# Optimization experiments

Measured on AMD Instinct MI355X. Metric: run time of the kernel, lower is better.

Reference implementation:

```python
import jax, jax.numpy as jnp
import numpy as np

BATCH = 2048
INPUT_DIM = 512
N = 8 ** 4  # reservoir_n ** reservoir_d = 4096
T = 16
NEG_SLOPE = 0.1
SPARSITY = 0.1  # fraction of nonzero entries in the pre-trained reservoir W


def setup_inputs() -> dict:
    key = jax.random.key(0)
    kx, kw, km = jax.random.split(key, 3)
    x = jax.random.normal(kx, (BATCH, INPUT_DIM), dtype=jnp.float32)
    # Sparse pre-trained reservoir weights; scale keeps spectral norm ~O(1)
    # so the T-step recurrence neither explodes nor vanishes.
    mask = (jax.random.uniform(km, (N, N)) < SPARSITY).astype(jnp.float32)
    W = jax.random.normal(kw, (N, N), dtype=jnp.float32) * mask / jnp.sqrt(SPARSITY * N)
    return {"x": x, "W": W}


def reference(x, W):
    # Pad input [B, input_dim] -> initial state S [B, N]
    S0 = jnp.pad(x, ((0, 0), (0, N - x.shape[1])))

    def step(S, _):
        S = jax.nn.leaky_relu(S @ W, negative_slope=NEG_SLOPE)
        return S, None

    S_final, _ = jax.lax.scan(step, S0, None, length=T)
    return S_final
```

## Files before the change

### kernel.cpp

```cpp
#include <hip/hip_runtime.h>


#define BATCH 2048
#define NDIM  4096
#define INDIM 512
#define BM 128
#define BN 128
#define BK 32

typedef _Float16 f16x8  __attribute__((ext_vector_type(8)));
typedef float    f32x16 __attribute__((ext_vector_type(16)));

__device__ __forceinline__ void async16(const void* gsrc, void* ldst) {
  const __attribute__((address_space(1))) unsigned int* g =
      (const __attribute__((address_space(1))) unsigned int*)gsrc;
  __attribute__((address_space(3))) unsigned int* l =
      (__attribute__((address_space(3))) unsigned int*)ldst;
  __builtin_amdgcn_global_load_lds(g, l, 16, 0, 0);
}

__global__ void prep_x(const float* __restrict__ x,
                       _Float16* __restrict__ Sh, _Float16* __restrict__ Sl) {
  size_t i = (size_t)blockIdx.x * 256 + threadIdx.x;
  int b = (int)(i >> 12);
  int n = (int)(i & (NDIM - 1));
  float v = (n < INDIM) ? x[(size_t)b * INDIM + n] : 0.0f;
  _Float16 h = (_Float16)v;
  Sh[i] = h;
  Sl[i] = (_Float16)(v - (float)h);
}

__global__ void prep_w(const float* __restrict__ W,
                       _Float16* __restrict__ Wth, _Float16* __restrict__ Wtl) {
  __shared__ float tile[32][33];
  int k0 = blockIdx.y * 32, n0 = blockIdx.x * 32;
  int tx = threadIdx.x, ty = threadIdx.y;
  for (int r = 0; r < 4; r++) {
    int k = k0 + ty + r * 8;
    tile[ty + r * 8][tx] = W[(size_t)k * NDIM + n0 + tx];
  }
  __syncthreads();
  for (int r = 0; r < 4; r++) {
    int n = n0 + ty + r * 8;
    float v = tile[tx][ty + r * 8] * 256.0f;
    _Float16 h = (_Float16)v;
    Wth[(size_t)n * NDIM + k0 + tx] = h;
    Wtl[(size_t)n * NDIM + k0 + tx] = (_Float16)(v - (float)h);
  }
}

#define READF(b, A, L, Bv, M)                          \
  do {                                                 \
    _Pragma("unroll") for (int i = 0; i < 2; i++)      \
    _Pragma("unroll") for (int s = 0; s < 2; s++) {    \
      A[i][s]  = *(const f16x8*)&sAh[b][oA[i][s]];     \
      L[i][s]  = *(const f16x8*)&sAl[b][oA[i][s]];     \
      Bv[i][s] = *(const f16x8*)&sBh[b][oB[i][s]];     \
      M[i][s]  = *(const f16x8*)&sBl[b][oB[i][s]];     \
    }                                                  \
  } while (0)

#define MFMAS(A, L, Bv, M)                                                                   \
  do {                                                                                       \
    _Pragma("unroll") for (int s = 0; s < 2; s++) {                                          \
      _Pragma("unroll") for (int j = 0; j < 2; j++)                                          \
      _Pragma("unroll") for (int i = 0; i < 2; i++)                                          \
        acc[i][j] = __builtin_amdgcn_mfma_f32_32x32x16_f16(A[i][s], Bv[j][s], acc[i][j], 0, 0, 0); \
      _Pragma("unroll") for (int j = 0; j < 2; j++)                                          \
      _Pragma("unroll") for (int i = 0; i < 2; i++)                                          \
        acc[i][j] = __builtin_amdgcn_mfma_f32_32x32x16_f16(L[i][s], Bv[j][s], acc[i][j], 0, 0, 0); \
      _Pragma("unroll") for (int j = 0; j < 2; j++)                                          \
      _Pragma("unroll") for (int i = 0; i < 2; i++)                                          \
        acc[i][j] = __builtin_amdgcn_mfma_f32_32x32x16_f16(A[i][s], M[j][s], acc[i][j], 0, 0, 0); \
    }                                                                                        \
  } while (0)

template <int MODE>
__global__ __launch_bounds__(256, 2) void step_kernel(
    const _Float16* __restrict__ Ah, const _Float16* __restrict__ Al,
    const _Float16* __restrict__ Bh, const _Float16* __restrict__ Bl,
    _Float16* __restrict__ Dh, _Float16* __restrict__ Dl,
    float* __restrict__ Dout, int k_len) {
  __shared__ _Float16 sAh[2][BM * BK];
  __shared__ _Float16 sAl[2][BM * BK];
  __shared__ _Float16 sBh[2][BN * BK];
  __shared__ _Float16 sBl[2][BN * BK];

  const int tid = threadIdx.x;
  const int lane = tid & 63;
  const int w = tid >> 6;
  const int wm = w >> 1, wn = w & 1;

  int id = blockIdx.x;
  int xcd = id & 7, local = id >> 3;
  int lr = local & 7, lc = local >> 3;
  const int bm = ((xcd & 1) * 8 + lr) * BM;
  const int bn = ((xcd >> 1) * 8 + lc) * BN;

  const int r31 = lane & 31;
  const int kh = lane >> 5;

  const int lane_off = (lane & 15) * 32 + (((lane >> 4) ^ ((lane >> 1) & 3)) * 8);

  int oA[2][2], oB[2][2];
#pragma unroll
  for (int i = 0; i < 2; i++)
#pragma unroll
    for (int s = 0; s < 2; s++) {
      oA[i][s] = (wm * 2 + i) * 1024 + s * 512 + lane_off;
      oB[i][s] = (wn * 2 + i) * 1024 + s * 512 + lane_off;
    }

  {
  }
  const int xsw = (lane & 3) ^ ((lane >> 3) & 3);
  const int srow = (lane >> 2) + ((xsw & 1) << 4);
  const int kc8 = (xsw >> 1) * 8;
  const size_t gA0 = (size_t)(bm + w * 32 + srow) * NDIM + kc8;
  const size_t gB0 = (size_t)(bn + w * 32 + srow) * NDIM + kc8;
  const int lo0 = w * 1024 + lane * 8;

  auto stage = [&](int kt, int b) {
    async16(Ah + gA0 + kt,      &sAh[b][lo0]);
    async16(Ah + gA0 + kt + 16, &sAh[b][lo0 + 512]);
    async16(Al + gA0 + kt,      &sAl[b][lo0]);
    async16(Al + gA0 + kt + 16, &sAl[b][lo0 + 512]);
    async16(Bh + gB0 + kt,      &sBh[b][lo0]);
    async16(Bh + gB0 + kt + 16, &sBh[b][lo0 + 512]);
    async16(Bl + gB0 + kt,      &sBl[b][lo0]);
    async16(Bl + gB0 + kt + 16, &sBl[b][lo0 + 512]);
  };

  f32x16 acc[2][2];
#pragma unroll
  for (int i = 0; i < 2; i++)
#pragma unroll
    for (int j = 0; j < 2; j++)
#pragma unroll
      for (int e = 0; e < 16; e++) acc[i][j][e] = 0.0f;

  f16x8 a0[2][2], l0[2][2], b0[2][2], m0[2][2];
  f16x8 a1[2][2], l1[2][2], b1[2][2], m1[2][2];

  const int nk = k_len / BK;

  stage(0 * BK, 0);
  stage(1 * BK, 1);
  __syncthreads();
  READF(0, a0, l0, b0, m0);
  __syncthreads();
  stage(2 * BK, 0);

  int it = 1;
  for (; it + 1 < nk; it += 2) {
    READF(1, a1, l1, b1, m1);
    MFMAS(a0, l0, b0, m0);
    __syncthreads();
    if (it + 2 < nk) stage((it + 2) * BK, 1);

    READF(0, a0, l0, b0, m0);
    MFMAS(a1, l1, b1, m1);
    __syncthreads();
    if (it + 3 < nk) stage((it + 3) * BK, 0);
  }
  READF(1, a1, l1, b1, m1);
  MFMAS(a0, l0, b0, m0);
  MFMAS(a1, l1, b1, m1);

  const float inv = 1.0f / 256.0f;
#pragma unroll
  for (int i = 0; i < 2; i++) {
#pragma unroll
    for (int j = 0; j < 2; j++) {
#pragma unroll
      for (int e = 0; e < 16; e++) {
        int r = bm + wm * 64 + i * 32 + (e & 3) + 8 * (e >> 2) + 4 * kh;
        int c = bn + wn * 64 + j * 32 + r31;
        float g = acc[i][j][e] * inv;
        float s = (g > 0.0f) ? g : 0.1f * g;
        if (MODE == 0) {
          _Float16 h = (_Float16)s;
          Dh[(size_t)r * NDIM + c] = h;
          Dl[(size_t)r * NDIM + c] = (_Float16)(s - (float)h);
        } else {
          Dout[(size_t)r * NDIM + c] = s;
        }
      }
    }
  }
}

extern "C" void kernel_launch(void* const* d_in, const int* in_sizes, int n_in,
                              void* d_out, int out_size, void* d_ws, size_t ws_size,
                              hipStream_t stream) {
  const float* x = (const float*)d_in[0];
  const float* W = (const float*)d_in[1];
  float* out = (float*)d_out;
  char* ws = (char*)d_ws;

  const size_t WT_BYTES = (size_t)NDIM * NDIM * 2;
  const size_t S_BYTES = (size_t)BATCH * NDIM * 2;
  _Float16* Wth = (_Float16*)ws;
  _Float16* Wtl = (_Float16*)(ws + WT_BYTES);
  _Float16* SAh = (_Float16*)(ws + 2 * WT_BYTES);
  _Float16* SAl = (_Float16*)(ws + 2 * WT_BYTES + S_BYTES);
  _Float16* SBh = (_Float16*)(ws + 2 * WT_BYTES + 2 * S_BYTES);
  _Float16* SBl = (_Float16*)(ws + 2 * WT_BYTES + 3 * S_BYTES);

  prep_x<<<(BATCH * NDIM) / 256, 256, 0, stream>>>(x, SAh, SAl);
  prep_w<<<dim3(NDIM / 32, NDIM / 32), dim3(32, 8), 0, stream>>>(W, Wth, Wtl);

  dim3 grid((NDIM / BN) * (BATCH / BM));
  for (int t = 1; t <= 16; t++) {
    const _Float16* ah = (t & 1) ? SAh : SBh;
    const _Float16* al = (t & 1) ? SAl : SBl;
    _Float16* dh = (t & 1) ? SBh : SAh;
    _Float16* dl = (t & 1) ? SBl : SAl;
    int klen = (t == 1) ? INDIM : NDIM;
    if (t < 16)
      step_kernel<0><<<grid, 256, 0, stream>>>(ah, al, Wth, Wtl, dh, dl, nullptr, klen);
    else
      step_kernel<1><<<grid, 256, 0, stream>>>(ah, al, Wth, Wtl, nullptr, nullptr, out, klen);
  }
}
```

Measured before the change: 2.924 ms.

## Store state and weights in pre-swizzled tiled layout for contiguous LDS staging

```diff
diff --git a/kernel.cpp b/kernel.cpp
--- a/kernel.cpp
+++ b/kernel.cpp
@@ -8,6 +8,7 @@
 #define BN 128
 #define BK 32
 
+typedef _Float16 f16x4  __attribute__((ext_vector_type(4)));
 typedef _Float16 f16x8  __attribute__((ext_vector_type(8)));
 typedef float    f32x16 __attribute__((ext_vector_type(16)));
 
@@ -17,6 +18,11 @@
   __attribute__((address_space(3))) unsigned int* l =
       (__attribute__((address_space(3))) unsigned int*)ldst;
   __builtin_amdgcn_global_load_lds(g, l, 16, 0, 0);
+}
+
+__device__ __forceinline__ int slot_of(int rho, int cb) {
+  int x = ((rho >> 4) & 1) | (cb << 1);
+  return ((rho & 15) << 2) | (x ^ ((rho >> 1) & 3));
 }
 
 __global__ void prep_x(const float* __restrict__ x,
@@ -26,27 +32,44 @@
   int n = (int)(i & (NDIM - 1));
   float v = (n < INDIM) ? x[(size_t)b * INDIM + n] : 0.0f;
   _Float16 h = (_Float16)v;
-  Sh[i] = h;
-  Sl[i] = (_Float16)(v - (float)h);
+  int rb = b >> 5, rho = b & 31;
+  int kt = n >> 5, cn = n & 31;
+  int chunk = cn >> 3, e = cn & 7;
+  int s = chunk >> 1, cb = chunk & 1;
+  int lp = slot_of(rho, cb);
+  size_t a = ((((size_t)rb * 128 + kt) * 2 + s) << 9) + lp * 8 + e;
+  Sh[a] = h;
+  Sl[a] = (_Float16)(v - (float)h);
 }
 
 __global__ void prep_w(const float* __restrict__ W,
                        _Float16* __restrict__ Wth, _Float16* __restrict__ Wtl) {
   __shared__ float tile[32][33];
-  int k0 = blockIdx.y * 32, n0 = blockIdx.x * 32;
+  int nb = blockIdx.x, ktb = blockIdx.y;
+  int k0 = ktb * 32, n0 = nb * 32;
+  int tid = threadIdx.y * 32 + threadIdx.x;
   int tx = threadIdx.x, ty = threadIdx.y;
   for (int r = 0; r < 4; r++) {
-    int k = k0 + ty + r * 8;
-    tile[ty + r * 8][tx] = W[(size_t)k * NDIM + n0 + tx];
+    int k = ty + r * 8;
+    tile[k][tx] = W[(size_t)(k0 + k) * NDIM + n0 + tx];
   }
   __syncthreads();
-  for (int r = 0; r < 4; r++) {
-    int n = n0 + ty + r * 8;
-    float v = tile[tx][ty + r * 8] * 256.0f;
+  int s = tid >> 7, lp = (tid >> 1) & 63, hh = tid & 1;
+  int x = (lp & 3) ^ ((lp >> 3) & 3);
+  int rho = (lp >> 2) + ((x & 1) << 4);
+  int cb = x >> 1;
+  int kbase = (2 * s + cb) * 8 + hh * 4;
+  f16x4 hi4, lo4;
+#pragma unroll
+  for (int q = 0; q < 4; q++) {
+    float v = tile[kbase + q][rho] * 256.0f;
     _Float16 h = (_Float16)v;
-    Wth[(size_t)n * NDIM + k0 + tx] = h;
-    Wtl[(size_t)n * NDIM + k0 + tx] = (_Float16)(v - (float)h);
-  }
+    hi4[q] = h;
+    lo4[q] = (_Float16)(v - (float)h);
+  }
+  size_t base = ((((size_t)nb * 128 + ktb) * 2 + s) << 9) + lp * 8 + hh * 4;
+  *(f16x4*)&Wth[base] = hi4;
+  *(f16x4*)&Wtl[base] = lo4;
 }
 
 #define READF(b, A, L, Bv, M)                          \
@@ -111,24 +134,22 @@
       oB[i][s] = (wn * 2 + i) * 1024 + s * 512 + lane_off;
     }
 
-  {
-  }
-  const int xsw = (lane & 3) ^ ((lane >> 3) & 3);
-  const int srow = (lane >> 2) + ((xsw & 1) << 4);
-  const int kc8 = (xsw >> 1) * 8;
-  const size_t gA0 = (size_t)(bm + w * 32 + srow) * NDIM + kc8;
-  const size_t gB0 = (size_t)(bn + w * 32 + srow) * NDIM + kc8;
-  const int lo0 = w * 1024 + lane * 8;
-
-  auto stage = [&](int kt, int b) {
-    async16(Ah + gA0 + kt,      &sAh[b][lo0]);
-    async16(Ah + gA0 + kt + 16, &sAh[b][lo0 + 512]);
-    async16(Al + gA0 + kt,      &sAl[b][lo0]);
-    async16(Al + gA0 + kt + 16, &sAl[b][lo0 + 512]);
-    async16(Bh + gB0 + kt,      &sBh[b][lo0]);
-    async16(Bh + gB0 + kt + 16, &sBh[b][lo0 + 512]);
-    async16(Bl + gB0 + kt,      &sBl[b][lo0]);
-    async16(Bl + gB0 + kt + 16, &sBl[b][lo0 + 512]);
+  const size_t rbA = (size_t)((bm >> 5) + w) * 128;
+  const size_t rbB = (size_t)((bn >> 5) + w) * 128;
+  const int l8 = lane * 8;
+  const int lo0 = w * 1024 + l8;
+
+  auto stage = [&](int ktI, int b) {
+    const size_t rA = (rbA + ktI) << 10;
+    const size_t rB = (rbB + ktI) << 10;
+    async16(Ah + rA + l8,       &sAh[b][lo0]);
+    async16(Ah + rA + 512 + l8, &sAh[b][lo0 + 512]);
+    async16(Al + rA + l8,       &sAl[b][lo0]);
+    async16(Al + rA + 512 + l8, &sAl[b][lo0 + 512]);
+    async16(Bh + rB + l8,       &sBh[b][lo0]);
+    async16(Bh + rB + 512 + l8, &sBh[b][lo0 + 512]);
+    async16(Bl + rB + l8,       &sBl[b][lo0]);
+    async16(Bl + rB + 512 + l8, &sBl[b][lo0 + 512]);
   };
 
   f32x16 acc[2][2];
@@ -144,45 +165,52 @@
 
   const int nk = k_len / BK;
 
-  stage(0 * BK, 0);
-  stage(1 * BK, 1);
+  stage(0, 0);
+  stage(1, 1);
   __syncthreads();
   READF(0, a0, l0, b0, m0);
   __syncthreads();
-  stage(2 * BK, 0);
+  stage(2, 0);
 
   int it = 1;
   for (; it + 1 < nk; it += 2) {
     READF(1, a1, l1, b1, m1);
     MFMAS(a0, l0, b0, m0);
     __syncthreads();
-    if (it + 2 < nk) stage((it + 2) * BK, 1);
+    if (it + 2 < nk) stage(it + 2, 1);
 
     READF(0, a0, l0, b0, m0);
     MFMAS(a1, l1, b1, m1);
     __syncthreads();
-    if (it + 3 < nk) stage((it + 3) * BK, 0);
+    if (it + 3 < nk) stage(it + 3, 0);
   }
   READF(1, a1, l1, b1, m1);
   MFMAS(a0, l0, b0, m0);
   MFMAS(a1, l1, b1, m1);
 
   const float inv = 1.0f / 256.0f;
+  const int chunk = r31 >> 3, ec = r31 & 7;
+  const int s2 = chunk >> 1, cb = chunk & 1;
 #pragma unroll
   for (int i = 0; i < 2; i++) {
 #pragma unroll
     for (int j = 0; j < 2; j++) {
 #pragma unroll
-      for (int e = 0; e < 16; e++) {
-        int r = bm + wm * 64 + i * 32 + (e & 3) + 8 * (e >> 2) + 4 * kh;
-        int c = bn + wn * 64 + j * 32 + r31;
-        float g = acc[i][j][e] * inv;
+      for (int u = 0; u < 16; u++) {
+        int rho = (u & 3) + 8 * (u >> 2) + 4 * kh;
+        float g = acc[i][j][u] * inv;
         float s = (g > 0.0f) ? g : 0.1f * g;
         if (MODE == 0) {
+          int rb = (bm >> 5) + wm * 2 + i;
+          int ktn = (bn >> 5) + wn * 2 + j;
+          int lp = slot_of(rho, cb);
+          size_t a = ((((size_t)rb * 128 + ktn) * 2 + s2) << 9) + lp * 8 + ec;
           _Float16 h = (_Float16)s;
-          Dh[(size_t)r * NDIM + c] = h;
-          Dl[(size_t)r * NDIM + c] = (_Float16)(s - (float)h);
+          Dh[a] = h;
+          Dl[a] = (_Float16)(s - (float)h);
         } else {
+          int r = bm + wm * 64 + i * 32 + rho;
+          int c = bn + wn * 64 + j * 32 + r31;
           Dout[(size_t)r * NDIM + c] = s;
         }
       }
```

Measured after the change: 2.572 ms. 12.0% less time.
